# Performance work log

Measured on AMD Instinct MI355X. Metric: run time of the kernel, lower is better.

## Reference

```python
import jax, jax.numpy as jnp
import numpy as np

N_NODES = 100000
N_EDGES = 600000
D = 128  # input_dim == output_dim (required by index_add into zeros_like(x) + residual)
EPS = 1e-5


def _linear_params(key, d_in, d_out):
    kw, kb = jax.random.split(key)
    bound = 1.0 / np.sqrt(d_in)
    w = jax.random.uniform(kw, (d_in, d_out), minval=-bound, maxval=bound, dtype=jnp.float32)
    b = jax.random.uniform(kb, (d_out,), minval=-bound, maxval=bound, dtype=jnp.float32)
    return w, b


def setup_inputs() -> dict:
    key = jax.random.key(0)
    ks = jax.random.split(key, 6)
    x = jax.random.normal(ks[0], (N_NODES, D), dtype=jnp.float32)
    edge_index = jax.random.randint(ks[1], (2, N_EDGES), 0, N_NODES, dtype=jnp.int32)
    w_m1, b_m1 = _linear_params(ks[2], 2 * D, D)
    w_m2, b_m2 = _linear_params(ks[3], D, D)
    w_u1, b_u1 = _linear_params(ks[4], 2 * D, D)
    w_u2, b_u2 = _linear_params(ks[5], D, D)
    gamma = jnp.ones((D,), dtype=jnp.float32)
    beta = jnp.zeros((D,), dtype=jnp.float32)
    return {
        "x": x, "edge_index": edge_index,
        "w_m1": w_m1, "b_m1": b_m1, "w_m2": w_m2, "b_m2": b_m2,
        "w_u1": w_u1, "b_u1": b_u1, "w_u2": w_u2, "b_u2": b_u2,
        "gamma": gamma, "beta": beta,
    }


def _layernorm(h, gamma, beta):
    mu = jnp.mean(h, axis=-1, keepdims=True)
    var = jnp.mean(jnp.square(h - mu), axis=-1, keepdims=True)
    return (h - mu) * jax.lax.rsqrt(var + EPS) * gamma + beta


def reference(x, edge_index, w_m1, b_m1, w_m2, b_m2, w_u1, b_u1, w_u2, b_u2, gamma, beta):
    row, col = edge_index[0], edge_index[1]
    # message MLP on concat of gathered endpoints: [E, 2D] -> [E, D]
    m_in = jnp.concatenate([x[row], x[col]], axis=-1)
    m = jax.nn.relu(m_in @ w_m1 + b_m1) @ w_m2 + b_m2
    # scatter-add messages to destination nodes (index_add along dim 0 with col)
    agg = jax.ops.segment_sum(m, col, num_segments=x.shape[0])
    # update MLP on [N, 2D] -> [N, D]
    u_in = jnp.concatenate([x, agg], axis=-1)
    h = jax.nn.relu(u_in @ w_u1 + b_u1) @ w_u2 + b_u2
    return _layernorm(h, gamma, beta) + x
```

## Files before the change

kernel.cpp:

```cpp
#include <hip/hip_runtime.h>
#include <hip/hip_bf16.h>
#include <stdint.h>

#define N_NODES 100000
#define N_EDGES 600000
#define D 128
#define EPS 1e-5f
#define SCAN_BS 512
#define ROW_MASK 0x1FFFF

#define PREP_BLOCKS 321
#define HIST_BLOCKS 2344
#define XF_BLOCKS   3125
#define SC_BLOCKS   9375
#define UPD_BLOCKS  3125

typedef __attribute__((ext_vector_type(8))) short short8;
typedef __attribute__((ext_vector_type(16))) float floatx16;


__device__ __forceinline__ uint32_t pack_bf16_rne(float lo, float hi) {
    uint32_t ul = __builtin_bit_cast(uint32_t, lo);
    uint32_t uh = __builtin_bit_cast(uint32_t, hi);
    ul += 0x7fffu + ((ul >> 16) & 1u);
    uh += 0x7fffu + ((uh >> 16) & 1u);
    return (ul >> 16) | (uh & 0xffff0000u);
}

__device__ __forceinline__ unsigned short f32_to_bf16_rne(float f) {
    uint32_t u = __builtin_bit_cast(uint32_t, f);
    u += 0x7fffu + ((u >> 16) & 1u);
    return (unsigned short)(u >> 16);
}

__device__ __forceinline__ float bflo(uint32_t a) { return __builtin_bit_cast(float, a << 16); }
__device__ __forceinline__ float bfhi(uint32_t a) { return __builtin_bit_cast(float, a & 0xffff0000u); }

__global__ void prep_hist(const float* __restrict__ w_m1, const float* __restrict__ w_u1,
                          const float* __restrict__ w_u2, const float* __restrict__ w_m2,
                          const float* __restrict__ b_m2,
                          unsigned short* __restrict__ wm1f, unsigned short* __restrict__ wu1tf,
                          unsigned short* __restrict__ wu2f, unsigned short* __restrict__ wcf,
                          float* __restrict__ vb,
                          const int* __restrict__ col, int* __restrict__ count,
                          int* __restrict__ rank) {
    if (blockIdx.x >= PREP_BLOCKS) {
        int e = (blockIdx.x - PREP_BLOCKS) * 256 + threadIdx.x;
        if (e < N_EDGES) rank[e] = atomicAdd(&count[col[e]], 1);
        return;
    }
    int idx = blockIdx.x * 256 + threadIdx.x;
    if (idx < 32768) {
        int j = idx & 7, lane = (idx >> 3) & 63, t = (idx >> 9) & 3, s = idx >> 11;
        int kk = s * 16 + ((lane >> 5) << 3) + j;
        wm1f[idx] = f32_to_bf16_rne(w_m1[kk * 128 + t * 32 + (lane & 31)]);
    } else if (idx < 49152) {
        int ii = idx - 32768;
        int j = ii & 7, lane = (ii >> 3) & 63, t = (ii >> 9) & 3, s = ii >> 11;
        int kk = s * 16 + ((lane >> 5) << 3) + j;
        wu1tf[ii] = f32_to_bf16_rne(w_u1[kk * 128 + t * 32 + (lane & 31)]);
    } else if (idx < 65536) {
        int ii = idx - 49152;
        int j = ii & 7, lane = (ii >> 3) & 63, t = (ii >> 9) & 3, s = ii >> 11;
        int kk = s * 16 + ((lane >> 5) << 3) + j;
        wu2f[ii] = f32_to_bf16_rne(w_u2[kk * 128 + t * 32 + (lane & 31)]);
    } else if (idx < 81920) {
        int ii = idx - 65536;
        int j = ii & 7, lane = (ii >> 3) & 63, t = (ii >> 9) & 3, s = ii >> 11;
        int kk = s * 16 + ((lane >> 5) << 3) + j;
        int nn = t * 32 + (lane & 31);
        float acc = 0.0f;
        for (int q = 0; q < 128; ++q)
            acc += w_m2[kk * 128 + q] * w_u1[(128 + q) * 128 + nn];
        wcf[ii] = f32_to_bf16_rne(acc);
    } else if (idx < 82048) {
        int nn = idx - 81920;
        float acc = 0.0f;
        for (int q = 0; q < 128; ++q)
            acc += b_m2[q] * w_u1[(128 + q) * 128 + nn];
        vb[nn] = acc;
    }
}

__global__ void scan_one(const int* __restrict__ count, int* __restrict__ base,
                         int* __restrict__ gcur) {
    __shared__ int tmp[SCAN_BS];
    __shared__ int bbase;
    int g = blockIdx.x * SCAN_BS + threadIdx.x;
    int v = (g < N_NODES) ? count[g] : 0;
    tmp[threadIdx.x] = v;
    __syncthreads();
    int acc = v;
#pragma unroll
    for (int off = 1; off < SCAN_BS; off <<= 1) {
        int add = (threadIdx.x >= off) ? tmp[threadIdx.x - off] : 0;
        __syncthreads();
        acc += add;
        tmp[threadIdx.x] = acc;
        __syncthreads();
    }
    if (threadIdx.x == SCAN_BS - 1) bbase = atomicAdd(gcur, acc);
    __syncthreads();
    if (g < N_NODES) base[g] = bbase + acc - v;
}

__launch_bounds__(64, 4)
__global__ void xform_scatter(const float* __restrict__ x, const short8* __restrict__ w1f,
                              const float* __restrict__ b1, unsigned short* __restrict__ xtb,
                              const int* __restrict__ row, const int* __restrict__ col,
                              const int* __restrict__ rank, const int* __restrict__ base,
                              int* __restrict__ srow) {
    if (blockIdx.x >= XF_BLOCKS) {
        int e = (blockIdx.x - XF_BLOCKS) * 64 + threadIdx.x;
        if (e < N_EDGES) {
            int c = col[e];
            int p = base[c] + rank[e];
            srow[p] = row[e] | ((c & 31) << 17);
        }
        return;
    }

    __shared__ __align__(16) short h1[32 * 136];
    const int lane = threadIdx.x;
    const int l31  = lane & 31;
    const int half = lane >> 5;
    short* hl = h1;

    const int nbase = blockIdx.x * 32;
    const int n = nbase + l31;
    const float* px = x + (size_t)n * D + half * 8;

    union { short8 v; uint32_t u[4]; } fa[8];
#pragma unroll
    for (int s = 0; s < 8; ++s) {
        const int off = s * 16;
        float4 a0 = *(const float4*)(px + off);
        float4 a1 = *(const float4*)(px + off + 4);
        fa[s].u[0] = pack_bf16_rne(a0.x, a0.y); fa[s].u[1] = pack_bf16_rne(a0.z, a0.w);
        fa[s].u[2] = pack_bf16_rne(a1.x, a1.y); fa[s].u[3] = pack_bf16_rne(a1.z, a1.w);
    }

#pragma unroll
    for (int p = 0; p < 2; ++p) {
        floatx16 acc[4];
#pragma unroll
        for (int t = 0; t < 4; ++t) acc[t] = (floatx16)0.0f;
#pragma unroll
        for (int s = 0; s < 8; ++s) {
#pragma unroll
            for (int t = 0; t < 4; ++t) {
                short8 wf = w1f[((p * 8 + s) * 4 + t) * 64 + lane];
                acc[t] = __builtin_amdgcn_mfma_f32_32x32x16_bf16(fa[s].v, wf, acc[t], 0, 0, 0);
            }
        }
#pragma unroll
        for (int t = 0; t < 4; ++t) {
            float bias = p ? b1[t * 32 + l31] : 0.0f;
#pragma unroll
            for (int r = 0; r < 16; ++r) {
                int m = (r & 3) + 8 * (r >> 2) + 4 * half;
                hl[m * 136 + t * 32 + l31] = (short)f32_to_bf16_rne(acc[t][r] + bias);
            }
        }
#pragma unroll
        for (int it = 0; it < 8; ++it) {
            int off = it * 512 + lane * 8;
            int r2 = off >> 7;
            int c2 = off & 127;
            short8 v = *(const short8*)(hl + r2 * 136 + c2);
            *(short8*)(xtb + (size_t)(nbase + r2) * 256 + p * 128 + c2) = v;
        }
    }
}

__launch_bounds__(64, 4)
__global__ void upd_kernel(const float* __restrict__ x, const uint32_t* __restrict__ xtb32,
                           const int* __restrict__ srowpk,
                           const int* __restrict__ base, const int* __restrict__ count,
                           const short8* __restrict__ wu1tf, const short8* __restrict__ wcf,
                           const short8* __restrict__ wu2f,
                           const float* __restrict__ b_u1, const float* __restrict__ vb,
                           const float* __restrict__ b_u2,
                           const float* __restrict__ gamma, const float* __restrict__ beta,
                           float* __restrict__ out) {
    __shared__ __align__(16) short h1[32 * 136];
    const int lane = threadIdx.x;
    const int l31  = lane & 31;
    const int half = lane >> 5;
    short* hl = h1;
    uint32_t* accu = (uint32_t*)hl;

    const int nbase = blockIdx.x * 32;
    const int nc = nbase + l31;

    const int b_l = base[nc];
    const int c_l = count[nc];
    const int ebeg = __shfl(b_l, 0);
    const int eend = __shfl(b_l, 31) + __shfl(c_l, 31);
    const float dgv = (float)c_l;

#pragma unroll
    for (int i = 0; i < 32; ++i) accu[i * 64 + lane] = 0;

    {
        float s_lo = 0.0f, s_hi = 0.0f;
        int curnib = -1;
        for (int t0 = ebeg; t0 < eend; t0 += 64) {
            const int nb = min(64, eend - t0);
            int pk = (lane < nb) ? srowpk[t0 + lane] : 0;
            for (int d = 0; d < nb; d += 8) {
                uint32_t av[8], bv[8];
                int nn[8];
#pragma unroll
                for (int k = 0; k < 8; ++k) {
                    int p = __shfl(pk, min(d + k, nb - 1));
                    int r = p & ROW_MASK;
                    nn[k] = p >> 17;
                    av[k] = xtb32[(size_t)r * 128 + lane];
                    bv[k] = xtb32[(size_t)(nbase + nn[k]) * 128 + 64 + lane];
                }
#pragma unroll
                for (int k = 0; k < 8; ++k) {
                    if (d + k < nb) {
                        float vlo = fmaxf(bflo(av[k]) + bflo(bv[k]), 0.0f);
                        float vhi = fmaxf(bfhi(av[k]) + bfhi(bv[k]), 0.0f);
                        if (nn[k] != curnib) {
                            if (curnib >= 0) accu[curnib * 64 + lane] = pack_bf16_rne(s_lo, s_hi);
                            curnib = nn[k]; s_lo = vlo; s_hi = vhi;
                        } else { s_lo += vlo; s_hi += vhi; }
                    }
                }
            }
        }
        if (curnib >= 0) accu[curnib * 64 + lane] = pack_bf16_rne(s_lo, s_hi);
    }

    const float* px = x + (size_t)nc * D + half * 8;

    floatx16 acc[4];
#pragma unroll
    for (int t = 0; t < 4; ++t) acc[t] = (floatx16)0.0f;

#pragma unroll
    for (int s = 0; s < 16; ++s) {
        union { short8 v; uint32_t u[4]; } fa;
        const short8* bf;
        if (s < 8) {
            const int off = s * 16;
            float4 a0 = *(const float4*)(px + off);
            float4 a1 = *(const float4*)(px + off + 4);
            fa.u[0] = pack_bf16_rne(a0.x, a0.y); fa.u[1] = pack_bf16_rne(a0.z, a0.w);
            fa.u[2] = pack_bf16_rne(a1.x, a1.y); fa.u[3] = pack_bf16_rne(a1.z, a1.w);
            bf = wu1tf + (s * 4) * 64;
        } else {
            fa.v = *(const short8*)((const short*)accu + l31 * 128 + (s - 8) * 16 + half * 8);
            bf = wcf + ((s - 8) * 4) * 64;
        }
#pragma unroll
        for (int t = 0; t < 4; ++t) {
            short8 wf = bf[t * 64 + lane];
            acc[t] = __builtin_amdgcn_mfma_f32_32x32x16_bf16(fa.v, wf, acc[t], 0, 0, 0);
        }
    }

    float bu1[4], vbt[4];
#pragma unroll
    for (int t = 0; t < 4; ++t) {
        bu1[t] = b_u1[t * 32 + l31];
        vbt[t] = vb[t * 32 + l31];
    }

#pragma unroll
    for (int r = 0; r < 16; ++r) {
        int m = (r & 3) + 8 * (r >> 2) + 4 * half;
        float dg = __shfl(dgv, m, 32);
#pragma unroll
        for (int t = 0; t < 4; ++t) {
            float v = fmaxf(acc[t][r] + bu1[t] + dg * vbt[t], 0.0f);
            hl[m * 136 + t * 32 + l31] = (short)f32_to_bf16_rne(v);
        }
    }

    floatx16 acc2[4];
#pragma unroll
    for (int t = 0; t < 4; ++t) acc2[t] = (floatx16)0.0f;

#pragma unroll
    for (int s = 0; s < 8; ++s) {
        short8 af = *(const short8*)(hl + l31 * 136 + s * 16 + half * 8);
#pragma unroll
        for (int t = 0; t < 4; ++t) {
            short8 wf = wu2f[(s * 4 + t) * 64 + lane];
            acc2[t] = __builtin_amdgcn_mfma_f32_32x32x16_bf16(af, wf, acc2[t], 0, 0, 0);
        }
    }

    float g4[4], be4[4], bias2[4];
#pragma unroll
    for (int t = 0; t < 4; ++t) {
        g4[t]    = gamma[t * 32 + l31];
        be4[t]   = beta[t * 32 + l31];
        bias2[t] = b_u2[t * 32 + l31];
    }

    float* hf = (float*)hl;
#pragma unroll
    for (int p = 0; p < 2; ++p) {
#pragma unroll
        for (int rr = 0; rr < 8; ++rr) {
            int r = p * 8 + rr;
            float hv[4];
            float s1 = 0.0f, s2 = 0.0f;
#pragma unroll
            for (int t = 0; t < 4; ++t) {
                hv[t] = acc2[t][r] + bias2[t];
                s1 += hv[t];
                s2 += hv[t] * hv[t];
            }
#pragma unroll
            for (int mask = 1; mask < 32; mask <<= 1) {
                s1 += __shfl_xor(s1, mask);
                s2 += __shfl_xor(s2, mask);
            }
            float mean = s1 * (1.0f / 128.0f);
            float var  = s2 * (1.0f / 128.0f) - mean * mean;
            float rs   = rsqrtf(var + EPS);
            int m = (r & 3) + 8 * (r >> 2) + 4 * half;
            int mrow = m - 16 * p;
#pragma unroll
            for (int t = 0; t < 4; ++t)
                hf[mrow * 132 + t * 32 + l31] = (hv[t] - mean) * rs * g4[t] + be4[t];
        }
#pragma unroll
        for (int it = 0; it < 8; ++it) {
            int q = it * 64 + lane;
            int r2 = q >> 5;
            int c4 = q & 31;
            int node = nbase + 16 * p + r2;
            float4 v = *(const float4*)(hf + r2 * 132 + c4 * 4);
            float4 xr = *(const float4*)(x + (size_t)node * D + c4 * 4);
            v.x += xr.x; v.y += xr.y; v.z += xr.z; v.w += xr.w;
            *(float4*)(out + (size_t)node * D + c4 * 4) = v;
        }
    }
}

extern "C" void kernel_launch(void* const* d_in, const int* in_sizes, int n_in,
                              void* d_out, int out_size, void* d_ws, size_t ws_size,
                              hipStream_t stream) {
    const float* x     = (const float*)d_in[0];
    const int*   edge  = (const int*)d_in[1];
    const float* w_m1  = (const float*)d_in[2];
    const float* b_m1  = (const float*)d_in[3];
    const float* w_m2  = (const float*)d_in[4];
    const float* b_m2  = (const float*)d_in[5];
    const float* w_u1  = (const float*)d_in[6];
    const float* b_u1  = (const float*)d_in[7];
    const float* w_u2  = (const float*)d_in[8];
    const float* b_u2  = (const float*)d_in[9];
    const float* gamma = (const float*)d_in[10];
    const float* beta  = (const float*)d_in[11];
    float* out = (float*)d_out;

    char* ws = (char*)d_ws;
    size_t off = 0;
    auto alloc = [&](size_t bytes) { void* p = ws + off; off = (off + bytes + 15) & ~(size_t)15; return p; };

    unsigned short* xtb   = (unsigned short*)alloc((size_t)N_NODES * 256 * 2);
    unsigned short* wm1f  = (unsigned short*)alloc(256 * 128 * 2);
    unsigned short* wu1tf = (unsigned short*)alloc(128 * 128 * 2);
    unsigned short* wcf   = (unsigned short*)alloc(128 * 128 * 2);
    unsigned short* wu2f  = (unsigned short*)alloc(128 * 128 * 2);
    float* vb    = (float*)alloc(128 * 4);
    int* count   = (int*)alloc((size_t)N_NODES * 4 + 16);
    int* gcur    = count + N_NODES;
    int* base    = (int*)alloc((size_t)N_NODES * 4);
    int* rank    = (int*)alloc((size_t)N_EDGES * 4);
    int* srow    = (int*)alloc((size_t)N_EDGES * 4);

    const int* rowi = edge;
    const int* coli = edge + N_EDGES;
    const int NB = (N_NODES + SCAN_BS - 1) / SCAN_BS;

    (void)hipMemsetAsync(count, 0, (size_t)N_NODES * 4 + 16, stream);

    prep_hist<<<PREP_BLOCKS + HIST_BLOCKS, 256, 0, stream>>>(
        w_m1, w_u1, w_u2, w_m2, b_m2, wm1f, wu1tf, wu2f, wcf, vb, coli, count, rank);

    scan_one<<<NB, SCAN_BS, 0, stream>>>(count, base, gcur);

    xform_scatter<<<XF_BLOCKS + SC_BLOCKS, 64, 0, stream>>>(
        x, (const short8*)wm1f, b_m1, xtb, rowi, coli, rank, base, srow);

    upd_kernel<<<UPD_BLOCKS, 64, 0, stream>>>(
        x, (const uint32_t*)xtb, srow, base, count,
        (const short8*)wu1tf, (const short8*)wcf, (const short8*)wu2f,
        b_u1, vb, b_u2, gamma, beta, out);
}
```

Baseline: 258.3 us.

## Split update gather into four 16-lane quarters with 16B loads and LDS-cached destination rows

The per-block edge aggregation now has each 16-lane quarter of the wavefront handle the edges of 8 destination nodes, loading 16-byte vectors of source rows instead of 4-byte per-lane loads. The destination-side transformed rows are staged once in shared memory instead of being re-read from global per edge, and the next batch of edge indices is prefetched. The edge-sort scatter processes four edges per thread with vectorised int4 loads, so fewer blocks are launched. The upd_kernel launch bound is relaxed to 2 to allow more registers, at the cost of occupancy and extra LDS.

```diff
diff --git a/kernel.cpp b/kernel.cpp
--- a/kernel.cpp
+++ b/kernel.cpp
@@ -12,7 +12,7 @@
 #define PREP_BLOCKS 321
 #define HIST_BLOCKS 2344
 #define XF_BLOCKS   3125
-#define SC_BLOCKS   9375
+#define SC_BLOCKS   2344
 #define UPD_BLOCKS  3125
 
 typedef __attribute__((ext_vector_type(8))) short short8;
@@ -111,11 +111,15 @@
                               const int* __restrict__ rank, const int* __restrict__ base,
                               int* __restrict__ srow) {
     if (blockIdx.x >= XF_BLOCKS) {
-        int e = (blockIdx.x - XF_BLOCKS) * 64 + threadIdx.x;
-        if (e < N_EDGES) {
-            int c = col[e];
-            int p = base[c] + rank[e];
-            srow[p] = row[e] | ((c & 31) << 17);
+        int e4 = (((blockIdx.x - XF_BLOCKS) * 64 + threadIdx.x) << 2);
+        if (e4 < N_EDGES) {
+            int4 r4 = *(const int4*)(row + e4);
+            int4 c4 = *(const int4*)(col + e4);
+            int4 k4 = *(const int4*)(rank + e4);
+            srow[base[c4.x] + k4.x] = r4.x | ((c4.x & 31) << 17);
+            srow[base[c4.y] + k4.y] = r4.y | ((c4.y & 31) << 17);
+            srow[base[c4.z] + k4.z] = r4.z | ((c4.z & 31) << 17);
+            srow[base[c4.w] + k4.w] = r4.w | ((c4.w & 31) << 17);
         }
         return;
     }
@@ -173,7 +177,7 @@
     }
 }
 
-__launch_bounds__(64, 4)
+__launch_bounds__(64, 2)
 __global__ void upd_kernel(const float* __restrict__ x, const uint32_t* __restrict__ xtb32,
                            const int* __restrict__ srowpk,
                            const int* __restrict__ base, const int* __restrict__ count,
@@ -184,9 +188,12 @@
                            const float* __restrict__ gamma, const float* __restrict__ beta,
                            float* __restrict__ out) {
     __shared__ __align__(16) short h1[32 * 136];
+    __shared__ __align__(16) uint32_t XBlds[32 * 64];
     const int lane = threadIdx.x;
     const int l31  = lane & 31;
     const int half = lane >> 5;
+    const int t    = lane & 15;
+    const int q16  = lane & 48;
     short* hl = h1;
     uint32_t* accu = (uint32_t*)hl;
 
@@ -195,51 +202,99 @@
 
     const int b_l = base[nc];
     const int c_l = count[nc];
-    const int ebeg = __shfl(b_l, 0);
-    const int eend = __shfl(b_l, 31) + __shfl(c_l, 31);
     const float dgv = (float)c_l;
 
-#pragma unroll
-    for (int i = 0; i < 32; ++i) accu[i * 64 + lane] = 0;
+    const int qsrc = q16 >> 1;
+    const int qbeg = __shfl(b_l, qsrc);
+    const int qend = __shfl(b_l, qsrc + 7) + __shfl(c_l, qsrc + 7);
+
+    int ncm = (qend - qbeg + 15) >> 4;
+    ncm = max(ncm, __shfl_xor(ncm, 16));
+    ncm = max(ncm, __shfl_xor(ncm, 32));
+
+#pragma unroll
+    for (int i = 0; i < 8; ++i) {
+        uint4 z; z.x = 0; z.y = 0; z.z = 0; z.w = 0;
+        *((uint4*)accu + i * 64 + lane) = z;
+    }
+
+#pragma unroll
+    for (int j = 0; j < 8; ++j) {
+        int fi = j * 64 + lane;
+        int i  = fi >> 4;
+        int k  = fi & 15;
+        uint4 v = *(const uint4*)(xtb32 + (size_t)(nbase + i) * 128 + 64 + (k << 2));
+        *((uint4*)XBlds + fi) = v;
+    }
 
     {
-        float s_lo = 0.0f, s_hi = 0.0f;
+        float sl0 = 0.f, sl1 = 0.f, sl2 = 0.f, sl3 = 0.f;
+        float sh0 = 0.f, sh1 = 0.f, sh2 = 0.f, sh3 = 0.f;
         int curnib = -1;
-        for (int t0 = ebeg; t0 < eend; t0 += 64) {
-            const int nb = min(64, eend - t0);
-            int pk = (lane < nb) ? srowpk[t0 + lane] : 0;
-            for (int d = 0; d < nb; d += 8) {
-                uint32_t av[8], bv[8];
-                int nn[8];
-#pragma unroll
-                for (int k = 0; k < 8; ++k) {
-                    int p = __shfl(pk, min(d + k, nb - 1));
-                    int r = p & ROW_MASK;
-                    nn[k] = p >> 17;
-                    av[k] = xtb32[(size_t)r * 128 + lane];
-                    bv[k] = xtb32[(size_t)(nbase + nn[k]) * 128 + 64 + lane];
-                }
-#pragma unroll
-                for (int k = 0; k < 8; ++k) {
-                    if (d + k < nb) {
-                        float vlo = fmaxf(bflo(av[k]) + bflo(bv[k]), 0.0f);
-                        float vhi = fmaxf(bfhi(av[k]) + bfhi(bv[k]), 0.0f);
-                        if (nn[k] != curnib) {
-                            if (curnib >= 0) accu[curnib * 64 + lane] = pack_bf16_rne(s_lo, s_hi);
-                            curnib = nn[k]; s_lo = vlo; s_hi = vhi;
-                        } else { s_lo += vlo; s_hi += vhi; }
+
+        auto flush = [&]() {
+            uint4 o;
+            o.x = pack_bf16_rne(sl0, sh0);
+            o.y = pack_bf16_rne(sl1, sh1);
+            o.z = pack_bf16_rne(sl2, sh2);
+            o.w = pack_bf16_rne(sl3, sh3);
+            *(uint4*)(accu + (curnib << 6) + (t << 2)) = o;
+        };
+
+        int pk = 0;
+        { int idx = qbeg + t; if (idx < qend) pk = srowpk[idx]; }
+
+        for (int c = 0; c < ncm; ++c) {
+            const int rem = qend - qbeg - (c << 4);
+
+            int pknext = 0;
+            { int idx = qbeg + ((c + 1) << 4) + t; if (idx < qend) pknext = srowpk[idx]; }
+
+            uint4 xt[16];
+#pragma unroll
+            for (int e = 0; e < 16; ++e) {
+                int pv = __shfl(pk, q16 + e);
+                uint4 z; z.x = 0; z.y = 0; z.z = 0; z.w = 0;
+                xt[e] = z;
+                if (e < rem)
+                    xt[e] = *(const uint4*)(xtb32 + (size_t)(pv & ROW_MASK) * 128 + (t << 2));
+            }
+
+#pragma unroll
+            for (int e = 0; e < 16; ++e) {
+                int pv = __shfl(pk, q16 + e);
+                if (e < rem) {
+                    int nib = pv >> 17;
+                    uint4 xb = *(const uint4*)(XBlds + (nib << 6) + (t << 2));
+                    float a0 = fmaxf(bflo(xt[e].x) + bflo(xb.x), 0.f);
+                    float b0 = fmaxf(bfhi(xt[e].x) + bfhi(xb.x), 0.f);
+                    float a1 = fmaxf(bflo(xt[e].y) + bflo(xb.y), 0.f);
+                    float b1 = fmaxf(bfhi(xt[e].y) + bfhi(xb.y), 0.f);
+                    float a2 = fmaxf(bflo(xt[e].z) + bflo(xb.z), 0.f);
+                    float b2 = fmaxf(bfhi(xt[e].z) + bfhi(xb.z), 0.f);
+                    float a3 = fmaxf(bflo(xt[e].w) + bflo(xb.w), 0.f);
+                    float b3 = fmaxf(bfhi(xt[e].w) + bfhi(xb.w), 0.f);
+                    if (nib != curnib) {
+                        if (curnib >= 0) flush();
+                        curnib = nib;
+                        sl0 = a0; sh0 = b0; sl1 = a1; sh1 = b1;
+                        sl2 = a2; sh2 = b2; sl3 = a3; sh3 = b3;
+                    } else {
+                        sl0 += a0; sh0 += b0; sl1 += a1; sh1 += b1;
+                        sl2 += a2; sh2 += b2; sl3 += a3; sh3 += b3;
                     }
                 }
             }
-        }
-        if (curnib >= 0) accu[curnib * 64 + lane] = pack_bf16_rne(s_lo, s_hi);
+            pk = pknext;
+        }
+        if (curnib >= 0) flush();
     }
 
     const float* px = x + (size_t)nc * D + half * 8;
 
     floatx16 acc[4];
 #pragma unroll
-    for (int t = 0; t < 4; ++t) acc[t] = (floatx16)0.0f;
+    for (int tt = 0; tt < 4; ++tt) acc[tt] = (floatx16)0.0f;
 
 #pragma unroll
     for (int s = 0; s < 16; ++s) {
@@ -257,17 +312,17 @@
             bf = wcf + ((s - 8) * 4) * 64;
         }
 #pragma unroll
-        for (int t = 0; t < 4; ++t) {
-            short8 wf = bf[t * 64 + lane];
-            acc[t] = __builtin_amdgcn_mfma_f32_32x32x16_bf16(fa.v, wf, acc[t], 0, 0, 0);
+        for (int tt = 0; tt < 4; ++tt) {
+            short8 wf = bf[tt * 64 + lane];
+            acc[tt] = __builtin_amdgcn_mfma_f32_32x32x16_bf16(fa.v, wf, acc[tt], 0, 0, 0);
         }
     }
 
     float bu1[4], vbt[4];
 #pragma unroll
-    for (int t = 0; t < 4; ++t) {
-        bu1[t] = b_u1[t * 32 + l31];
-        vbt[t] = vb[t * 32 + l31];
+    for (int tt = 0; tt < 4; ++tt) {
+        bu1[tt] = b_u1[tt * 32 + l31];
+        vbt[tt] = vb[tt * 32 + l31];
     }
 
 #pragma unroll
@@ -275,32 +330,32 @@
         int m = (r & 3) + 8 * (r >> 2) + 4 * half;
         float dg = __shfl(dgv, m, 32);
 #pragma unroll
-        for (int t = 0; t < 4; ++t) {
-            float v = fmaxf(acc[t][r] + bu1[t] + dg * vbt[t], 0.0f);
-            hl[m * 136 + t * 32 + l31] = (short)f32_to_bf16_rne(v);
+        for (int tt = 0; tt < 4; ++tt) {
+            float v = fmaxf(acc[tt][r] + bu1[tt] + dg * vbt[tt], 0.0f);
+            hl[m * 136 + tt * 32 + l31] = (short)f32_to_bf16_rne(v);
         }
     }
 
     floatx16 acc2[4];
 #pragma unroll
-    for (int t = 0; t < 4; ++t) acc2[t] = (floatx16)0.0f;
+    for (int tt = 0; tt < 4; ++tt) acc2[tt] = (floatx16)0.0f;
 
 #pragma unroll
     for (int s = 0; s < 8; ++s) {
         short8 af = *(const short8*)(hl + l31 * 136 + s * 16 + half * 8);
 #pragma unroll
-        for (int t = 0; t < 4; ++t) {
-            short8 wf = wu2f[(s * 4 + t) * 64 + lane];
-            acc2[t] = __builtin_amdgcn_mfma_f32_32x32x16_bf16(af, wf, acc2[t], 0, 0, 0);
+        for (int tt = 0; tt < 4; ++tt) {
+            short8 wf = wu2f[(s * 4 + tt) * 64 + lane];
+            acc2[tt] = __builtin_amdgcn_mfma_f32_32x32x16_bf16(af, wf, acc2[tt], 0, 0, 0);
         }
     }
 
     float g4[4], be4[4], bias2[4];
 #pragma unroll
-    for (int t = 0; t < 4; ++t) {
-        g4[t]    = gamma[t * 32 + l31];
-        be4[t]   = beta[t * 32 + l31];
-        bias2[t] = b_u2[t * 32 + l31];
+    for (int tt = 0; tt < 4; ++tt) {
+        g4[tt]    = gamma[tt * 32 + l31];
+        be4[tt]   = beta[tt * 32 + l31];
+        bias2[tt] = b_u2[tt * 32 + l31];
     }
 
     float* hf = (float*)hl;
@@ -312,10 +367,10 @@
             float hv[4];
             float s1 = 0.0f, s2 = 0.0f;
 #pragma unroll
-            for (int t = 0; t < 4; ++t) {
-                hv[t] = acc2[t][r] + bias2[t];
-                s1 += hv[t];
-                s2 += hv[t] * hv[t];
+            for (int tt = 0; tt < 4; ++tt) {
+                hv[tt] = acc2[tt][r] + bias2[tt];
+                s1 += hv[tt];
+                s2 += hv[tt] * hv[tt];
             }
 #pragma unroll
             for (int mask = 1; mask < 32; mask <<= 1) {
@@ -328,14 +383,14 @@
             int m = (r & 3) + 8 * (r >> 2) + 4 * half;
             int mrow = m - 16 * p;
 #pragma unroll
-            for (int t = 0; t < 4; ++t)
-                hf[mrow * 132 + t * 32 + l31] = (hv[t] - mean) * rs * g4[t] + be4[t];
+            for (int tt = 0; tt < 4; ++tt)
+                hf[mrow * 132 + tt * 32 + l31] = (hv[tt] - mean) * rs * g4[tt] + be4[tt];
         }
 #pragma unroll
         for (int it = 0; it < 8; ++it) {
-            int q = it * 64 + lane;
-            int r2 = q >> 5;
-            int c4 = q & 31;
+            int qq = it * 64 + lane;
+            int r2 = qq >> 5;
+            int c4 = qq & 31;
             int node = nbase + 16 * p + r2;
             float4 v = *(const float4*)(hf + r2 * 132 + c4 * 4);
             float4 xr = *(const float4*)(x + (size_t)node * D + c4 * 4);
```

New measurement: 256.3 us. About the same (-0.8%).
